# Performance work log

Hardware: AMD Instinct MI355X
Metric: run time of the kernel (lower is better)

Reference implementation:

```python
import jax, jax.numpy as jnp
import numpy as np

S, C = 4096, 12            # words per sentence, chars per word
V, NC = 50000, 26          # word vocab, char vocab
E, EC = 1024, 256          # word / char embedding dims
H, HC = 1024, 256          # word / char LSTM hidden dims
T = 64                     # tagset size


def _lstm_step(W_ih, W_hh, b_ih, b_hh, carry, x):
    # PyTorch LSTM gate order: i, f, g, o
    h, c = carry
    gates = x @ W_ih.T + h @ W_hh.T + b_ih + b_hh
    i, f, g, o = jnp.split(gates, 4, axis=-1)
    c = jax.nn.sigmoid(f) * c + jax.nn.sigmoid(i) * jnp.tanh(g)
    h = jax.nn.sigmoid(o) * jnp.tanh(c)
    return (h, c), h


def setup_inputs() -> dict:
    key = jax.random.key(0)
    ks = jax.random.split(key, 16)
    s = 0.02
    return {
        "char_idx": jax.random.randint(ks[0], (S, C), 0, NC),
        "word_idx": jax.random.randint(ks[1], (S,), 0, V),
        "W_emb_word": jax.random.normal(ks[2], (V, E), jnp.float32) * s,
        "W_emb_char": jax.random.normal(ks[3], (NC, EC), jnp.float32) * s,
        "W_ih_c": jax.random.normal(ks[4], (4 * HC, EC), jnp.float32) * s,
        "W_hh_c": jax.random.normal(ks[5], (4 * HC, HC), jnp.float32) * s,
        "b_ih_c": jnp.zeros((4 * HC,), jnp.float32),
        "b_hh_c": jnp.zeros((4 * HC,), jnp.float32),
        "W_ih": jax.random.normal(ks[6], (4 * H, E + HC), jnp.float32) * s,
        "W_hh": jax.random.normal(ks[7], (4 * H, H), jnp.float32) * s,
        "b_ih": jnp.zeros((4 * H,), jnp.float32),
        "b_hh": jnp.zeros((4 * H,), jnp.float32),
        "W_tag": jax.random.normal(ks[8], (T, H), jnp.float32) * s,
        "b_tag": jnp.zeros((T,), jnp.float32),
    }


def reference(char_idx, word_idx, W_emb_word, W_emb_char,
              W_ih_c, W_hh_c, b_ih_c, b_hh_c,
              W_ih, W_hh, b_ih, b_hh, W_tag, b_tag):
    # --- char-level LSTM, batched over all S words at once ---
    char_x = W_emb_char[char_idx]                     # [S, C, EC]
    carry0 = (jnp.zeros((S, HC), char_x.dtype), jnp.zeros((S, HC), char_x.dtype))
    step_c = lambda carry, x: _lstm_step(W_ih_c, W_hh_c, b_ih_c, b_hh_c, carry, x)
    (h_char, _), _ = jax.lax.scan(step_c, carry0, jnp.swapaxes(char_x, 0, 1))  # h_char: [S, HC]

    # --- word-level LSTM over the sentence (batch 1) ---
    word_emb = W_emb_word[word_idx]                   # [S, E]
    x = jnp.concatenate([word_emb, h_char], axis=-1)  # [S, E+HC]
    carry0w = (jnp.zeros((H,), x.dtype), jnp.zeros((H,), x.dtype))
    step_w = lambda carry, xt: _lstm_step(W_ih, W_hh, b_ih, b_hh, carry, xt)
    _, hs = jax.lax.scan(step_w, carry0w, x)          # hs: [S, H]

    tag_space = hs @ W_tag.T + b_tag                  # [S, T]
    return jax.nn.log_softmax(tag_space, axis=1)
```

## Files before the change

kernel.cpp:

```cpp
#include <hip/hip_runtime.h>
#include <hip/hip_bf16.h>

#define SLEN 4096
#define CLEN 12
#define ECD  256
#define HCD  256
#define ED   1024
#define HD   1024
#define TD   64
#define NSLOT 32
#define POLL_LIMIT 2048

typedef unsigned  uv4 __attribute__((ext_vector_type(4)));
typedef __attribute__((ext_vector_type(8))) short bf16x8;
typedef __attribute__((ext_vector_type(4))) float f32x4;

#if defined(__has_builtin)
#if __has_builtin(__builtin_amdgcn_sdot4)
#define HAVE_SDOT4 1
#endif
#if __has_builtin(__builtin_amdgcn_perm)
#define HAVE_PERM 1
#endif
#endif

#ifdef HAVE_PERM
#define PERM2(hi, lo) __builtin_amdgcn_perm((unsigned)(hi), (unsigned)(lo), 0x05040100u)
#else
#define PERM2(hi, lo) ((((unsigned)(lo)) & 0xFFFFu) | (((unsigned)(hi)) << 16))
#endif

__device__ __forceinline__ float sigmoidf_(float x) { return 1.f / (1.f + __expf(-x)); }
__device__ __forceinline__ float tanh_fast(float x) {
    float ax = fabsf(x);
    float e = __expf(2.f * ax);
    float t = 1.f - 2.f / (e + 1.f);
    return copysignf(t, x);
}
__device__ __forceinline__ unsigned short bf16r(float f) {
    unsigned u = __float_as_uint(f);
    return (unsigned short)((u + 0x7FFFu + ((u >> 16) & 1u)) >> 16);
}

__global__ __launch_bounds__(256) void prep_all(
    const float* __restrict__ Wih,  unsigned short* __restrict__ Wihb,
    const float* __restrict__ Wec,  const float* __restrict__ Wihc,
    const float* __restrict__ bihc, const float* __restrict__ bhhc,
    float* __restrict__ table,
    const float* __restrict__ Whhc, unsigned short* __restrict__ Wt,
    const float* __restrict__ Wtag, unsigned short* __restrict__ Wtagb,
    unsigned* __restrict__ hdata, int* __restrict__ xcd_ctr)
{
    const int b = blockIdx.x, tid = threadIdx.x;
    if (b < 2560) {
        int i = b * 256 + tid;
        const float4* s = reinterpret_cast<const float4*>(Wih + (size_t)i * 8);
        float4 a = s[0], b2 = s[1];
        unsigned short o[8] = { bf16r(a.x), bf16r(a.y), bf16r(a.z), bf16r(a.w),
                                bf16r(b2.x), bf16r(b2.y), bf16r(b2.z), bf16r(b2.w) };
        *reinterpret_cast<uint4*>(Wihb + (size_t)i * 8) = *reinterpret_cast<uint4*>(o);
    } else if (b < 2664) {
        int id = (b - 2560) * 256 + tid;
        if (id < 26 * 1024) {
            int c = id >> 10, rp = id & 1023;
            int u = rp >> 2, g = rp & 3, row = g * 256 + u;
            const float4* a = reinterpret_cast<const float4*>(Wec + (size_t)c * 256);
            const float4* bb = reinterpret_cast<const float4*>(Wihc + (size_t)row * 256);
            float acc = 0.f;
            #pragma unroll 16
            for (int k = 0; k < 64; ++k) {
                float4 av = a[k], bv = bb[k];
                acc += av.x * bv.x + av.y * bv.y + av.z * bv.z + av.w * bv.w;
            }
            table[id] = acc + bihc[row] + bhhc[row];
        }
    } else if (b < 2792) {
        int id = (b - 2664) * 256 + tid;
        int C = id >> 5, kg = id & 31;
        int h = C >> 9, rem = C & 511, g = rem >> 7, ul = rem & 127;
        int row = g * 256 + h * 128 + ul;
        const float4* sv = reinterpret_cast<const float4*>(
            Whhc + (size_t)row * 256 + kg * 8);
        float4 a = sv[0], b2 = sv[1];
        unsigned short o[8] = { bf16r(a.x), bf16r(a.y), bf16r(a.z), bf16r(a.w),
                                bf16r(b2.x), bf16r(b2.y), bf16r(b2.z), bf16r(b2.w) };
        *reinterpret_cast<uint4*>(Wt + (size_t)(kg * 1024 + C) * 8) =
            *reinterpret_cast<uint4*>(o);
    } else if (b < 2824) {
        int i = (b - 2792) * 256 + tid;
        const float4* s = reinterpret_cast<const float4*>(Wtag + (size_t)i * 8);
        float4 a = s[0], b2 = s[1];
        unsigned short o[8] = { bf16r(a.x), bf16r(a.y), bf16r(a.z), bf16r(a.w),
                                bf16r(b2.x), bf16r(b2.y), bf16r(b2.z), bf16r(b2.w) };
        *reinterpret_cast<uint4*>(Wtagb + (size_t)i * 8) = *reinterpret_cast<uint4*>(o);
    } else if (b < 2856) {
        hdata[(b - 2824) * 256 + tid] = 0xFFFF0000u;
    } else {
        if (tid < 8) xcd_ctr[tid] = 0;
    }
}

__global__ __launch_bounds__(256) void build_Xw(
    const int* __restrict__ word_idx, const float* __restrict__ Wemb,
    const unsigned short* __restrict__ h_cb, unsigned short* __restrict__ Xw)
{
    int id = blockIdx.x * 256 + threadIdx.x;
    int row = id / 160, c8 = id % 160;
    int k = c8 * 8;
    uint4 outv;
    if (k < 1024) {
        const float4* sv = reinterpret_cast<const float4*>(
            Wemb + (size_t)word_idx[row] * 1024 + k);
        float4 a = sv[0], b = sv[1];
        unsigned short o[8] = { bf16r(a.x), bf16r(a.y), bf16r(a.z), bf16r(a.w),
                                bf16r(b.x), bf16r(b.y), bf16r(b.z), bf16r(b.w) };
        outv = *reinterpret_cast<uint4*>(o);
    } else {
        outv = *reinterpret_cast<const uint4*>(h_cb + (size_t)row * 256 + (k - 1024));
    }
    *reinterpret_cast<uint4*>(Xw + (size_t)row * 1280 + k) = outv;
}

__global__ __launch_bounds__(256) void char_fused(
    const int* __restrict__ char_idx,
    const unsigned short* __restrict__ Wt,
    const float* __restrict__ table,
    unsigned short* __restrict__ h_cb)
{
    __shared__ unsigned short hA[2][8192];
    __shared__ int cidx_s[32 * CLEN];

    const int tid  = threadIdx.x;
    const int lane = tid & 63;
    const int wv   = tid >> 6;
    const int fr   = lane & 15;
    const int fkq  = lane >> 4;
    const int w0   = blockIdx.x * 32;

    for (int e = tid; e < 32 * CLEN; e += 256)
        cidx_s[e] = char_idx[(w0 + (e / CLEN)) * CLEN + (e % CLEN)];
    {
        uint4 z; z.x = z.y = z.z = z.w = 0u;
        for (int e = tid; e < 1024; e += 256)
            *reinterpret_cast<uint4*>(&hA[0][e * 8]) = z;
    }
    __syncthreads();

    float cst[32];
    #pragma unroll
    for (int i = 0; i < 32; ++i) cst[i] = 0.f;

    for (int t = 0; t < CLEN; ++t) {
        const int cur = t & 1, nxt = cur ^ 1;
        #pragma unroll
        for (int h = 0; h < 2; ++h) {
            f32x4 acc[2][8];
            #pragma unroll
            for (int m = 0; m < 2; ++m)
                #pragma unroll
                for (int i = 0; i < 8; ++i) acc[m][i] = f32x4{0.f, 0.f, 0.f, 0.f};

            #pragma unroll
            for (int k0i = 0; k0i < 8; ++k0i) {
                const int kg = k0i * 4 + fkq;
                bf16x8 af[2];
                #pragma unroll
                for (int m = 0; m < 2; ++m) {
                    const int row = m * 16 + fr;
                    af[m] = *reinterpret_cast<const bf16x8*>(
                        &hA[cur][row * 256 + ((kg ^ ((row & 7) << 2)) << 3)]);
                }
                #pragma unroll
                for (int i = 0; i < 8; ++i) {
                    const int T = wv + (i << 2);
                    const int col = h * 512 + T * 16 + fr;
                    const bf16x8 bf = *reinterpret_cast<const bf16x8*>(
                        Wt + (size_t)(kg * 1024 + col) * 8);
                    acc[0][i] = __builtin_amdgcn_mfma_f32_16x16x32_bf16(
                        af[0], bf, acc[0][i], 0, 0, 0);
                    acc[1][i] = __builtin_amdgcn_mfma_f32_16x16x32_bf16(
                        af[1], bf, acc[1][i], 0, 0, 0);
                }
            }

            #pragma unroll
            for (int m = 0; m < 2; ++m) {
                #pragma unroll
                for (int r = 0; r < 4; ++r) {
                    const int wl = m * 16 + (lane >> 4) * 4 + r;
                    const int ci = cidx_s[wl * CLEN + t];
                    #pragma unroll
                    for (int ab = 0; ab < 2; ++ab) {
                        const int u = h * 128 + (wv + 4 * ab) * 16 + fr;
                        const float4 tv = *reinterpret_cast<const float4*>(
                            table + (size_t)ci * 1024 + u * 4);
                        const int cix = ((h * 2 + m) * 2 + ab) * 4 + r;
                        const float gi_ = acc[m][0 + ab][r] + tv.x;
                        const float gf_ = acc[m][2 + ab][r] + tv.y;
                        const float gg_ = acc[m][4 + ab][r] + tv.z;
                        const float go_ = acc[m][6 + ab][r] + tv.w;
                        const float i_ = sigmoidf_(gi_), f_ = sigmoidf_(gf_);
                        const float g_ = tanh_fast(gg_), o_ = sigmoidf_(go_);
                        const float cn = f_ * cst[cix] + i_ * g_;
                        cst[cix] = cn;
                        const unsigned short hb = bf16r(o_ * tanh_fast(cn));
                        const int chn = u >> 3;
                        hA[nxt][wl * 256 + ((chn ^ ((wl & 7) << 2)) << 3) + (u & 7)] = hb;
                    }
                }
            }
        }
        __syncthreads();
    }

    for (int e = tid; e < 1024; e += 256) {
        const int w = e >> 5, ch = e & 31;
        uint4 v = *reinterpret_cast<uint4*>(
            &hA[0][w * 256 + ((ch ^ ((w & 7) << 2)) << 3)]);
        *reinterpret_cast<uint4*>(h_cb + (size_t)(w0 + w) * 256 + ch * 8) = v;
    }
}

__global__ __launch_bounds__(256) void gemm_bf16_bt(
    const unsigned short* __restrict__ A, const unsigned short* __restrict__ B,
    const float* __restrict__ bias0, const float* __restrict__ bias1,
    float* __restrict__ C, int M, int N, int K)
{
    __shared__ unsigned short As[128 * 64];
    __shared__ unsigned short Bs[128 * 64];
    const int tid  = threadIdx.x;
    const int lane = tid & 63;
    const int wm = (tid >> 6) >> 1, wn = (tid >> 6) & 1;
    const int fr = lane & 15, fk = lane >> 4;
    const int n0 = blockIdx.x * 128;
    const int m0 = blockIdx.y * 128;

    uint4 ar[4], br[4];
    int rowi[4], kci[4];
    #pragma unroll
    for (int c = 0; c < 4; ++c) {
        int ch = c * 256 + tid;
        rowi[c] = ch >> 3; kci[c] = ch & 7;
    }

    auto load_tiles = [&](int k0) {
        #pragma unroll
        for (int c = 0; c < 4; ++c) {
            ar[c] = *reinterpret_cast<const uint4*>(
                A + (size_t)(m0 + rowi[c]) * K + k0 + kci[c] * 8);
            br[c] = *reinterpret_cast<const uint4*>(
                B + (size_t)(n0 + rowi[c]) * K + k0 + kci[c] * 8);
        }
    };

    f32x4 acc[4][4];
    #pragma unroll
    for (int i = 0; i < 4; ++i)
        #pragma unroll
        for (int j = 0; j < 4; ++j) acc[i][j] = f32x4{0.f, 0.f, 0.f, 0.f};

    load_tiles(0);
    for (int k0 = 0; k0 < K; k0 += 64) {
        __syncthreads();
        #pragma unroll
        for (int c = 0; c < 4; ++c) {
            int sw = kci[c] ^ (rowi[c] & 7);
            *reinterpret_cast<uint4*>(&As[rowi[c] * 64 + sw * 8]) = ar[c];
            *reinterpret_cast<uint4*>(&Bs[rowi[c] * 64 + sw * 8]) = br[c];
        }
        __syncthreads();
        if (k0 + 64 < K) load_tiles(k0 + 64);
        #pragma unroll
        for (int ks = 0; ks < 2; ++ks) {
            bf16x8 af[4], bfr[4];
            #pragma unroll
            for (int i = 0; i < 4; ++i) {
                int ra = wm * 64 + i * 16 + fr;
                af[i] = *reinterpret_cast<const bf16x8*>(
                    &As[ra * 64 + (((ks * 4 + fk) ^ (ra & 7)) << 3)]);
                int rb = wn * 64 + i * 16 + fr;
                bfr[i] = *reinterpret_cast<const bf16x8*>(
                    &Bs[rb * 64 + (((ks * 4 + fk) ^ (rb & 7)) << 3)]);
            }
            #pragma unroll
            for (int i = 0; i < 4; ++i)
                #pragma unroll
                for (int j = 0; j < 4; ++j)
                    acc[i][j] = __builtin_amdgcn_mfma_f32_16x16x32_bf16(
                        af[i], bfr[j], acc[i][j], 0, 0, 0);
        }
    }

    const int colb = n0 + wn * 64 + fr;
    float bsum[4];
    #pragma unroll
    for (int j = 0; j < 4; ++j) bsum[j] = bias0[colb + j * 16] + bias1[colb + j * 16];
    #pragma unroll
    for (int i = 0; i < 4; ++i) {
        int row0 = m0 + wm * 64 + i * 16 + fk * 4;
        #pragma unroll
        for (int j = 0; j < 4; ++j) {
            int col = colb + j * 16;
            #pragma unroll
            for (int r = 0; r < 4; ++r)
                C[(size_t)(row0 + r) * N + col] = acc[i][j][r] + bsum[j];
        }
    }
}

__global__ __launch_bounds__(256, 1) void word_rec(
    const float* __restrict__ precomp, const float* __restrict__ W_hh,
    unsigned* __restrict__ hs_b, unsigned* hdata, int* xcd_ctr)
{
    const int tid  = threadIdx.x;
    const int v    = tid >> 6;
    const int lane = tid & 63;
    const int q    = lane >> 5;
    const int m    = lane & 31;
    const int j    = lane & 7;

    __shared__ int s_vals[2];
    if (tid == 0) {
        unsigned xcc;
        asm volatile("s_getreg_b32 %0, hwreg(HW_REG_XCC_ID)" : "=s"(xcc));
        xcc &= 7u;
        s_vals[0] = (int)xcc;
        s_vals[1] = atomicAdd(&xcd_ctr[xcc], 1);
    }
    __syncthreads();
    const int xcc  = s_vals[0];
    const int slot = s_vals[1];
    if (slot >= NSLOT) return;

    const int base_u = slot * 32 + v * 8;
    unsigned* hdata_x = hdata + xcc * 1024;

    int   wq[16][8];
    float scl[16];
    #pragma unroll
    for (int r = 0; r < 16; ++r) {
        const int grow = (2 * q + (r >> 3)) * 1024 + base_u + (r & 7);
        const float4* rp = reinterpret_cast<const float4*>(
            W_hh + (size_t)grow * 1024 + 32 * m);
        float wv_[32];
        float mx = 0.f;
        #pragma unroll
        for (int d = 0; d < 8; ++d) {
            float4 f = rp[d];
            wv_[4*d+0] = f.x; wv_[4*d+1] = f.y; wv_[4*d+2] = f.z; wv_[4*d+3] = f.w;
            mx = fmaxf(mx, fmaxf(fmaxf(fabsf(f.x), fabsf(f.y)),
                                 fmaxf(fabsf(f.z), fabsf(f.w))));
        }
        mx = fmaxf(mx, __shfl_xor(mx, 1));
        mx = fmaxf(mx, __shfl_xor(mx, 2));
        mx = fmaxf(mx, __shfl_xor(mx, 4));
        mx = fmaxf(mx, __shfl_xor(mx, 8));
        mx = fmaxf(mx, __shfl_xor(mx, 16));
        const float inv = (mx > 0.f) ? (127.f / mx) : 0.f;
        scl[r] = mx * (1.f / (127.f * 127.f));
        #pragma unroll
        for (int d = 0; d < 8; ++d) {
            int b0 = (int)rintf(wv_[4*d+0] * inv) & 255;
            int b1 = (int)rintf(wv_[4*d+1] * inv) & 255;
            int b2 = (int)rintf(wv_[4*d+2] * inv) & 255;
            int b3 = (int)rintf(wv_[4*d+3] * inv) & 255;
            wq[r][d] = b0 | (b1 << 8) | (b2 << 16) | (b3 << 24);
        }
    }

#ifdef HAVE_SDOT4
    #define DOT4(a, b, c) __builtin_amdgcn_sdot4((a), (b), (c), false)
#else
    #define DOT4(a, b, c) ({ int _d; \
        asm("v_dot4_i32_i8 %0, %1, %2, %3" : "=v"(_d) : "v"(a), "v"(b), "v"(c)); _d; })
#endif

    float c_reg = 0.f;

    for (int t = 0; t < SLEN; ++t) {
        const int pp = (t + 1) & 1;
        const int pc = t & 1;

        float pre0 = 0.f, pre1 = 0.f, pre2 = 0.f, pre3 = 0.f;
        if (lane < 8) {
            const float* pr = precomp + (size_t)t * 4096 + base_u + j;
            pre0 = pr[0]; pre1 = pr[1024]; pre2 = pr[2048]; pre3 = pr[3072];
        }

        int hq[8];
        if (t > 0) {
            const unsigned tw = ((unsigned)(t - 1)) << 16;
            const unsigned* dp = hdata_x + pp * 512 + 16 * m;
            uv4 w0_, w1_, w2_, w3_;
            int it = 0; bool dead = false;
            for (;;) {
                asm volatile(
                    "global_load_dwordx4 %0, %4, off sc0\n\t"
                    "global_load_dwordx4 %1, %4, off offset:16 sc0\n\t"
                    "global_load_dwordx4 %2, %4, off offset:32 sc0\n\t"
                    "global_load_dwordx4 %3, %4, off offset:48 sc0\n\t"
                    "s_waitcnt vmcnt(0)"
                    : "=&v"(w0_), "=&v"(w1_), "=&v"(w2_), "=&v"(w3_)
                    : "v"(dp) : "memory");
                unsigned bad =
                    (w0_.x ^ tw) | (w0_.y ^ tw) | (w0_.z ^ tw) | (w0_.w ^ tw) |
                    (w1_.x ^ tw) | (w1_.y ^ tw) | (w1_.z ^ tw) | (w1_.w ^ tw) |
                    (w2_.x ^ tw) | (w2_.y ^ tw) | (w2_.z ^ tw) | (w2_.w ^ tw) |
                    (w3_.x ^ tw) | (w3_.y ^ tw) | (w3_.z ^ tw) | (w3_.w ^ tw);
                if (__all((bad & 0xFFFF0000u) == 0u)) break;
                if (++it > POLL_LIMIT) { dead = true; break; }
            }
            if (dead) return;
            hq[0] = (int)PERM2(w0_.y, w0_.x);
            hq[1] = (int)PERM2(w0_.w, w0_.z);
            hq[2] = (int)PERM2(w1_.y, w1_.x);
            hq[3] = (int)PERM2(w1_.w, w1_.z);
            hq[4] = (int)PERM2(w2_.y, w2_.x);
            hq[5] = (int)PERM2(w2_.w, w2_.z);
            hq[6] = (int)PERM2(w3_.y, w3_.x);
            hq[7] = (int)PERM2(w3_.w, w3_.z);
        } else {
            #pragma unroll
            for (int i = 0; i < 8; ++i) hq[i] = 0;
        }

        float self = 0.f;
        #pragma unroll
        for (int r = 0; r < 16; ++r) {
            int a0 = 0, a1 = 0;
            #pragma unroll
            for (int d = 0; d < 4; ++d) {
                a0 = DOT4(wq[r][d],     hq[d],     a0);
                a1 = DOT4(wq[r][4 + d], hq[4 + d], a1);
            }
            int s = a0 + a1;
            s += __shfl_xor(s, 1);  s += __shfl_xor(s, 2);
            s += __shfl_xor(s, 4);  s += __shfl_xor(s, 8);
            s += __shfl_xor(s, 16);
            self = ((lane & 31) == r) ? (float)s * scl[r] : self;
        }

        const float gi = __shfl(self, j);
        const float gf = __shfl(self, 8 + j);
        const float gg = __shfl(self, 32 + j);
        const float go = __shfl(self, 40 + j);

        float h = 0.f;
        if (lane < 8) {
            const float i_ = sigmoidf_(gi + pre0);
            const float f_ = sigmoidf_(gf + pre1);
            const float g_ = tanh_fast(gg + pre2);
            const float o_ = sigmoidf_(go + pre3);
            c_reg = f_ * c_reg + i_ * g_;
            h = o_ * tanh_fast(c_reg);
        }

        const float hn = __shfl_down(h, 1);
        int qv = (int)rintf(fminf(fmaxf(h * 127.f, -127.f), 127.f));
        const int qn = __shfl(qv, lane | 1);
        if (lane < 8 && (lane & 1) == 0) {
            unsigned pb = (unsigned)bf16r(h) | ((unsigned)bf16r(hn) << 16);
            hs_b[(size_t)t * 512 + (base_u >> 1) + (lane >> 1)] = pb;
            unsigned pk = ((unsigned)t << 16) | ((unsigned)(qn & 255) << 8)
                        | (unsigned)(qv & 255);
            unsigned* dpw = hdata_x + pc * 512 + slot * 16 + v * 4 + (lane >> 1);
            asm volatile("global_store_dword %0, %1, off sc0"
                         :: "v"(dpw), "v"(pk) : "memory");
        }
    }
    #undef DOT4
}

__global__ __launch_bounds__(256) void tag_mfma(
    const unsigned short* __restrict__ A,
    const unsigned short* __restrict__ B,
    const float* __restrict__ btag, float* __restrict__ out)
{
    __shared__ unsigned short As[128 * 64];
    __shared__ unsigned short Bs[64 * 64];
    __shared__ float ts[128 * 65];

    const int tid  = threadIdx.x;
    const int lane = tid & 63;
    const int wm = (tid >> 6) >> 1, wn = (tid >> 6) & 1;
    const int fr = lane & 15, fk = lane >> 4;
    const int m0 = blockIdx.x * 128;

    uint4 ar[4], br[2];
    int rowa[4], kca[4], rowb[2], kcb[2];
    #pragma unroll
    for (int c = 0; c < 4; ++c) {
        int ch = c * 256 + tid;
        rowa[c] = ch >> 3; kca[c] = ch & 7;
    }
    #pragma unroll
    for (int c = 0; c < 2; ++c) {
        int ch = c * 256 + tid;
        rowb[c] = ch >> 3; kcb[c] = ch & 7;
    }

    auto load_tiles = [&](int k0) {
        #pragma unroll
        for (int c = 0; c < 4; ++c)
            ar[c] = *reinterpret_cast<const uint4*>(
                A + (size_t)(m0 + rowa[c]) * 1024 + k0 + kca[c] * 8);
        #pragma unroll
        for (int c = 0; c < 2; ++c)
            br[c] = *reinterpret_cast<const uint4*>(
                B + (size_t)rowb[c] * 1024 + k0 + kcb[c] * 8);
    };

    f32x4 acc[4][2];
    #pragma unroll
    for (int i = 0; i < 4; ++i)
        #pragma unroll
        for (int j = 0; j < 2; ++j) acc[i][j] = f32x4{0.f, 0.f, 0.f, 0.f};

    load_tiles(0);
    for (int k0 = 0; k0 < 1024; k0 += 64) {
        __syncthreads();
        #pragma unroll
        for (int c = 0; c < 4; ++c) {
            int sw = kca[c] ^ (rowa[c] & 7);
            *reinterpret_cast<uint4*>(&As[rowa[c] * 64 + sw * 8]) = ar[c];
        }
        #pragma unroll
        for (int c = 0; c < 2; ++c) {
            int sw = kcb[c] ^ (rowb[c] & 7);
            *reinterpret_cast<uint4*>(&Bs[rowb[c] * 64 + sw * 8]) = br[c];
        }
        __syncthreads();
        if (k0 + 64 < 1024) load_tiles(k0 + 64);
        #pragma unroll
        for (int ks = 0; ks < 2; ++ks) {
            bf16x8 af[4], bfr[2];
            #pragma unroll
            for (int i = 0; i < 4; ++i) {
                int ra = wm * 64 + i * 16 + fr;
                af[i] = *reinterpret_cast<const bf16x8*>(
                    &As[ra * 64 + (((ks * 4 + fk) ^ (ra & 7)) << 3)]);
            }
            #pragma unroll
            for (int j = 0; j < 2; ++j) {
                int rb = wn * 32 + j * 16 + fr;
                bfr[j] = *reinterpret_cast<const bf16x8*>(
                    &Bs[rb * 64 + (((ks * 4 + fk) ^ (rb & 7)) << 3)]);
            }
            #pragma unroll
            for (int i = 0; i < 4; ++i)
                #pragma unroll
                for (int j = 0; j < 2; ++j)
                    acc[i][j] = __builtin_amdgcn_mfma_f32_16x16x32_bf16(
                        af[i], bfr[j], acc[i][j], 0, 0, 0);
        }
    }

    #pragma unroll
    for (int i = 0; i < 4; ++i) {
        int row0 = wm * 64 + i * 16 + fk * 4;
        #pragma unroll
        for (int j = 0; j < 2; ++j) {
            int col = wn * 32 + j * 16 + fr;
            float bt = btag[col];
            #pragma unroll
            for (int r = 0; r < 4; ++r)
                ts[(row0 + r) * 65 + col] = acc[i][j][r] + bt;
        }
    }
    __syncthreads();

    if (tid < 128) {
        const float* rowp = ts + tid * 65;
        float mx = rowp[0];
        #pragma unroll 16
        for (int c = 1; c < 64; ++c) mx = fmaxf(mx, rowp[c]);
        float ssum = 0.f;
        #pragma unroll 16
        for (int c = 0; c < 64; ++c) ssum += __expf(rowp[c] - mx);
        const float lse = mx + logf(ssum);
        float* op = out + (size_t)(m0 + tid) * 64;
        #pragma unroll 16
        for (int c = 0; c < 64; ++c) op[c] = rowp[c] - lse;
    }
}

extern "C" void kernel_launch(void* const* d_in, const int* in_sizes, int n_in,
                              void* d_out, int out_size, void* d_ws, size_t ws_size,
                              hipStream_t stream)
{
    const int*   char_idx = (const int*)  d_in[0];
    const int*   word_idx = (const int*)  d_in[1];
    const float* Wemb     = (const float*)d_in[2];
    const float* Wec      = (const float*)d_in[3];
    const float* Wihc     = (const float*)d_in[4];
    const float* Whhc     = (const float*)d_in[5];
    const float* bihc     = (const float*)d_in[6];
    const float* bhhc     = (const float*)d_in[7];
    const float* Wih      = (const float*)d_in[8];
    const float* Whh      = (const float*)d_in[9];
    const float* bih      = (const float*)d_in[10];
    const float* bhh      = (const float*)d_in[11];
    const float* Wtag     = (const float*)d_in[12];
    const float* btag     = (const float*)d_in[13];
    float* out = (float*)d_out;

    char* w = (char*)d_ws;
    float*          precomp = (float*)w;            w += (size_t)SLEN * 4096 * 4;
    unsigned short* Wihb    = (unsigned short*)w;   w += (size_t)4096 * 1280 * 2;
    unsigned short* Xw      = (unsigned short*)w;   w += (size_t)4096 * 1280 * 2;
    unsigned*       hs_b    = (unsigned*)w;         w += (size_t)SLEN * 512 * 4;
    unsigned short* h_cb    = (unsigned short*)w;   w += (size_t)SLEN * HCD * 2;
    unsigned short* Wt      = (unsigned short*)w;   w += (size_t)32 * 1024 * 8 * 2;
    float*          table   = (float*)w;            w += 26 * 1024 * 4 + 1920;
    unsigned short* Wtagb   = (unsigned short*)w;   w += (size_t)64 * 1024 * 2;
    unsigned*       hdata   = (unsigned*)w;         w += 8 * 1024 * 4;
    int*            xcd_ctr = (int*)w;

    prep_all<<<2857, 256, 0, stream>>>(Wih, Wihb, Wec, Wihc, bihc, bhhc, table,
                                       Whhc, Wt, Wtag, Wtagb, hdata, xcd_ctr);

    char_fused<<<128, 256, 0, stream>>>(char_idx, Wt, table, h_cb);

    build_Xw<<<SLEN * 160 / 256, 256, 0, stream>>>(word_idx, Wemb, h_cb, Xw);
    gemm_bf16_bt<<<dim3(32, 32), 256, 0, stream>>>(
        Xw, Wihb, bih, bhh, precomp, SLEN, 4096, 1280);

    word_rec<<<256, 256, 0, stream>>>(precomp, Whh, hs_b, hdata, xcd_ctr);

    tag_mfma<<<32, 256, 0, stream>>>(
        (const unsigned short*)hs_b, Wtagb, btag, out);
}
```

Baseline: 981.1 us.

## Fold Xw build into prep kernel and use direct global-to-LDS loads in GEMM

The word-embedding gather and bf16 conversion move into the prep_all kernel, and the char LSTM writes its hidden state straight into the Xw columns. This removes the build_Xw launch and the h_cb intermediate buffer. The input-projection GEMM now loads tiles with global_load_lds, storing the XOR swizzle in the source address. That drops the register round-trip and LDS store instructions, but it also removes the software prefetch of the next tile, so the load latency is no longer overlapped with MFMA work.

```diff
diff --git a/kernel.cpp b/kernel.cpp
--- a/kernel.cpp
+++ b/kernel.cpp
@@ -30,6 +30,11 @@
 #define PERM2(hi, lo) ((((unsigned)(lo)) & 0xFFFFu) | (((unsigned)(hi)) << 16))
 #endif
 
+#define GLOAD_LDS16(g, l)                                                    \
+    __builtin_amdgcn_global_load_lds(                                        \
+        (const __attribute__((address_space(1))) void*)(g),                  \
+        (__attribute__((address_space(3))) void*)(l), 16, 0, 0)
+
 __device__ __forceinline__ float sigmoidf_(float x) { return 1.f / (1.f + __expf(-x)); }
 __device__ __forceinline__ float tanh_fast(float x) {
     float ax = fabsf(x);
@@ -49,7 +54,9 @@
     float* __restrict__ table,
     const float* __restrict__ Whhc, unsigned short* __restrict__ Wt,
     const float* __restrict__ Wtag, unsigned short* __restrict__ Wtagb,
-    unsigned* __restrict__ hdata, int* __restrict__ xcd_ctr)
+    unsigned* __restrict__ hdata, int* __restrict__ xcd_ctr,
+    const int* __restrict__ word_idx, const float* __restrict__ Wemb,
+    unsigned short* __restrict__ Xw)
 {
     const int b = blockIdx.x, tid = threadIdx.x;
     if (b < 2560) {
@@ -95,37 +102,27 @@
         *reinterpret_cast<uint4*>(Wtagb + (size_t)i * 8) = *reinterpret_cast<uint4*>(o);
     } else if (b < 2856) {
         hdata[(b - 2824) * 256 + tid] = 0xFFFF0000u;
+    } else if (b < 4904) {
+        int id = (b - 2856) * 256 + tid;
+        int row = id >> 7, c8 = id & 127;
+        int k = c8 * 8;
+        const float4* sv = reinterpret_cast<const float4*>(
+            Wemb + (size_t)word_idx[row] * 1024 + k);
+        float4 a = sv[0], b2 = sv[1];
+        unsigned short o[8] = { bf16r(a.x), bf16r(a.y), bf16r(a.z), bf16r(a.w),
+                                bf16r(b2.x), bf16r(b2.y), bf16r(b2.z), bf16r(b2.w) };
+        *reinterpret_cast<uint4*>(Xw + (size_t)row * 1280 + k) =
+            *reinterpret_cast<uint4*>(o);
     } else {
         if (tid < 8) xcd_ctr[tid] = 0;
     }
-}
-
-__global__ __launch_bounds__(256) void build_Xw(
-    const int* __restrict__ word_idx, const float* __restrict__ Wemb,
-    const unsigned short* __restrict__ h_cb, unsigned short* __restrict__ Xw)
-{
-    int id = blockIdx.x * 256 + threadIdx.x;
-    int row = id / 160, c8 = id % 160;
-    int k = c8 * 8;
-    uint4 outv;
-    if (k < 1024) {
-        const float4* sv = reinterpret_cast<const float4*>(
-            Wemb + (size_t)word_idx[row] * 1024 + k);
-        float4 a = sv[0], b = sv[1];
-        unsigned short o[8] = { bf16r(a.x), bf16r(a.y), bf16r(a.z), bf16r(a.w),
-                                bf16r(b.x), bf16r(b.y), bf16r(b.z), bf16r(b.w) };
-        outv = *reinterpret_cast<uint4*>(o);
-    } else {
-        outv = *reinterpret_cast<const uint4*>(h_cb + (size_t)row * 256 + (k - 1024));
-    }
-    *reinterpret_cast<uint4*>(Xw + (size_t)row * 1280 + k) = outv;
 }
 
 __global__ __launch_bounds__(256) void char_fused(
     const int* __restrict__ char_idx,
     const unsigned short* __restrict__ Wt,
     const float* __restrict__ table,
-    unsigned short* __restrict__ h_cb)
+    unsigned short* __restrict__ Xw)
 {
     __shared__ unsigned short hA[2][8192];
     __shared__ int cidx_s[32 * CLEN];
@@ -217,7 +214,8 @@
         const int w = e >> 5, ch = e & 31;
         uint4 v = *reinterpret_cast<uint4*>(
             &hA[0][w * 256 + ((ch ^ ((w & 7) << 2)) << 3)]);
-        *reinterpret_cast<uint4*>(h_cb + (size_t)(w0 + w) * 256 + ch * 8) = v;
+        *reinterpret_cast<uint4*>(
+            Xw + (size_t)(w0 + w) * 1280 + 1024 + ch * 8) = v;
     }
 }
 
@@ -230,46 +228,39 @@
     __shared__ unsigned short Bs[128 * 64];
     const int tid  = threadIdx.x;
     const int lane = tid & 63;
-    const int wm = (tid >> 6) >> 1, wn = (tid >> 6) & 1;
+    const int wv   = tid >> 6;
+    const int wm = wv >> 1, wn = wv & 1;
     const int fr = lane & 15, fk = lane >> 4;
     const int n0 = blockIdx.x * 128;
     const int m0 = blockIdx.y * 128;
 
-    uint4 ar[4], br[4];
-    int rowi[4], kci[4];
+    int srcA[4], srcB[4];
+    int ldsb[4];
     #pragma unroll
     for (int c = 0; c < 4; ++c) {
-        int ch = c * 256 + tid;
-        rowi[c] = ch >> 3; kci[c] = ch & 7;
-    }
-
-    auto load_tiles = [&](int k0) {
+        int ch = c * 256 + wv * 64 + lane;
+        int row = ch >> 3, chunk = ch & 7;
+        int swc = chunk ^ (row & 7);
+        srcA[c] = (m0 + row) * K + swc * 8;
+        srcB[c] = (n0 + row) * K + swc * 8;
+        ldsb[c] = (c * 256 + wv * 64) * 8;
+    }
+
+    f32x4 acc[4][4];
+    #pragma unroll
+    for (int i = 0; i < 4; ++i)
+        #pragma unroll
+        for (int j = 0; j < 4; ++j) acc[i][j] = f32x4{0.f, 0.f, 0.f, 0.f};
+
+    for (int k0 = 0; k0 < K; k0 += 64) {
+        if (k0 > 0) __syncthreads();
         #pragma unroll
         for (int c = 0; c < 4; ++c) {
-            ar[c] = *reinterpret_cast<const uint4*>(
-                A + (size_t)(m0 + rowi[c]) * K + k0 + kci[c] * 8);
-            br[c] = *reinterpret_cast<const uint4*>(
-                B + (size_t)(n0 + rowi[c]) * K + k0 + kci[c] * 8);
-        }
-    };
-
-    f32x4 acc[4][4];
-    #pragma unroll
-    for (int i = 0; i < 4; ++i)
-        #pragma unroll
-        for (int j = 0; j < 4; ++j) acc[i][j] = f32x4{0.f, 0.f, 0.f, 0.f};
-
-    load_tiles(0);
-    for (int k0 = 0; k0 < K; k0 += 64) {
+            GLOAD_LDS16(A + srcA[c] + k0, As + ldsb[c]);
+            GLOAD_LDS16(B + srcB[c] + k0, Bs + ldsb[c]);
+        }
+        asm volatile("s_waitcnt vmcnt(0)" ::: "memory");
         __syncthreads();
-        #pragma unroll
-        for (int c = 0; c < 4; ++c) {
-            int sw = kci[c] ^ (rowi[c] & 7);
-            *reinterpret_cast<uint4*>(&As[rowi[c] * 64 + sw * 8]) = ar[c];
-            *reinterpret_cast<uint4*>(&Bs[rowi[c] * 64 + sw * 8]) = br[c];
-        }
-        __syncthreads();
-        if (k0 + 64 < K) load_tiles(k0 + 64);
         #pragma unroll
         for (int ks = 0; ks < 2; ++ks) {
             bf16x8 af[4], bfr[4];
@@ -609,19 +600,18 @@
     unsigned short* Wihb    = (unsigned short*)w;   w += (size_t)4096 * 1280 * 2;
     unsigned short* Xw      = (unsigned short*)w;   w += (size_t)4096 * 1280 * 2;
     unsigned*       hs_b    = (unsigned*)w;         w += (size_t)SLEN * 512 * 4;
-    unsigned short* h_cb    = (unsigned short*)w;   w += (size_t)SLEN * HCD * 2;
     unsigned short* Wt      = (unsigned short*)w;   w += (size_t)32 * 1024 * 8 * 2;
     float*          table   = (float*)w;            w += 26 * 1024 * 4 + 1920;
     unsigned short* Wtagb   = (unsigned short*)w;   w += (size_t)64 * 1024 * 2;
     unsigned*       hdata   = (unsigned*)w;         w += 8 * 1024 * 4;
     int*            xcd_ctr = (int*)w;
 
-    prep_all<<<2857, 256, 0, stream>>>(Wih, Wihb, Wec, Wihc, bihc, bhhc, table,
-                                       Whhc, Wt, Wtag, Wtagb, hdata, xcd_ctr);
-
-    char_fused<<<128, 256, 0, stream>>>(char_idx, Wt, table, h_cb);
-
-    build_Xw<<<SLEN * 160 / 256, 256, 0, stream>>>(word_idx, Wemb, h_cb, Xw);
+    prep_all<<<4905, 256, 0, stream>>>(Wih, Wihb, Wec, Wihc, bihc, bhhc, table,
+                                       Whhc, Wt, Wtag, Wtagb, hdata, xcd_ctr,
+                                       word_idx, Wemb, Xw);
+
+    char_fused<<<128, 256, 0, stream>>>(char_idx, Wt, table, Xw);
+
     gemm_bf16_bt<<<dim3(32, 32), 256, 0, stream>>>(
         Xw, Wihb, bih, bhh, precomp, SLEN, 4096, 1280);
 
```

Result: faster. 842.5 us, median of 2 (-14.1%).
